# Kernel optimization log

Measured on AMD Instinct MI355X. Metric: run time of the kernel, lower is better.

The kernel has to match this reference:

```python
import jax, jax.numpy as jnp
import numpy as np

B, L, D = 4, 4096, 1024  # batch, seq_len, d_model


def setup_inputs() -> dict:
    key = jax.random.key(0)
    k0, k1, k2 = jax.random.split(key, 3)
    x = jax.random.normal(k0, (B, L, D), dtype=jnp.float32)
    # Dense(d_model*3) applied to x: kernel [D, 3D], bias [3D]
    W_proj = jax.random.normal(k1, (D, 3 * D), dtype=jnp.float32) / np.sqrt(D)
    b_proj = jnp.zeros((3 * D,), dtype=jnp.float32)
    # Output Dense(d_model): kernel [D, D], bias [D]
    W_out = jax.random.normal(k2, (D, D), dtype=jnp.float32) / np.sqrt(D)
    b_out = jnp.zeros((D,), dtype=jnp.float32)
    return {"x": x, "W_proj": W_proj, "b_proj": b_proj,
            "W_out": W_out, "b_out": b_out,
            "layer_idx": 0, "num_layers": 12}


def reference(x, W_proj, b_proj, W_out, b_out, layer_idx, num_layers):
    # x: [B, L, D] -> x_proj: [B, L, 3D]
    x_proj = jnp.einsum('bld,de->ble', x, W_proj) + b_proj
    gate_input, forget_input, output_gate = jnp.split(x_proj, 3, axis=-1)
    # NOTE: in the source, forget_gate / input_gate / k / v / the lax.scan
    # recurrence are defined but never used to produce the output (dead code).
    # The live path is exactly:
    out = gate_input * jax.nn.sigmoid(output_gate)          # [B, L, D]
    out = jnp.einsum('bld,de->ble', out, W_out) + b_out     # [B, L, D]
    # Dropout is deterministic (training=False) -> identity.
    return out
```

## Files before the change

### kernel.cpp

```cpp
#include <hip/hip_runtime.h>
#include <hip/hip_bf16.h>


#define MTOT 16384
#define DM   1024
#define MEG  (1024 * 1024)

typedef __bf16 bf16x8 __attribute__((ext_vector_type(8)));
typedef float  f32x4  __attribute__((ext_vector_type(4)));

#define AS1 __attribute__((address_space(1)))
#define AS3 __attribute__((address_space(3)))

static __device__ __forceinline__ void async_load16(const void* g, void* l) {
    __builtin_amdgcn_global_load_lds((const AS1 void*)g, (AS3 void*)l, 16, 0, 0);
}

static __device__ __forceinline__ unsigned short f2bf(float f) {
    __hip_bfloat16 h = __float2bfloat16(f);
    return *(unsigned short*)&h;
}

__global__ __launch_bounds__(256)
void conv_x(const float* __restrict__ x, unsigned short* __restrict__ dst) {
    const size_t i = ((size_t)blockIdx.x * 256 + threadIdx.x) * 8;
    const f32x4 a = *(const f32x4*)(x + i);
    const f32x4 b = *(const f32x4*)(x + i + 4);
    __align__(16) unsigned short o[8];
    o[0] = f2bf(a[0]); o[1] = f2bf(a[1]); o[2] = f2bf(a[2]); o[3] = f2bf(a[3]);
    o[4] = f2bf(b[0]); o[5] = f2bf(b[1]); o[6] = f2bf(b[2]); o[7] = f2bf(b[3]);
    *(uint4*)(dst + i) = *(const uint4*)o;
}

__global__ void transpose_w(const float* __restrict__ Wproj, const float* __restrict__ Wout,
                            unsigned short* __restrict__ dst0) {
    __shared__ unsigned short t[32][33];
    const int z = blockIdx.z;
    const float* src;
    unsigned short* dst;
    int ld, coff;
    if (z == 0)      { src = Wproj; ld = 3072; coff = 0;    dst = dst0; }
    else if (z == 1) { src = Wproj; ld = 3072; coff = 2048; dst = dst0 + MEG; }
    else             { src = Wout;  ld = 1024; coff = 0;    dst = dst0 + 2 * MEG; }
    const int k0 = blockIdx.x * 32;
    const int n0 = blockIdx.y * 32;
    const int tx = threadIdx.x, ty = threadIdx.y;
    for (int i = ty; i < 32; i += 8)
        t[i][tx] = f2bf(src[(size_t)(k0 + i) * ld + coff + n0 + tx]);
    __syncthreads();
    for (int i = ty; i < 32; i += 8)
        dst[(size_t)(n0 + i) * DM + k0 + tx] = t[tx][i];
}

__global__ __launch_bounds__(512)
void gemm1_fused(const unsigned short* __restrict__ X,
                 const unsigned short* __restrict__ WgT,
                 const unsigned short* __restrict__ WoT,
                 const float* __restrict__ bproj,
                 unsigned short* __restrict__ Hlo,
                 unsigned short* __restrict__ Hhi) {
    __shared__ __align__(16) unsigned short sA[2][256 * 64];
    __shared__ __align__(16) unsigned short sB[2][256 * 64];

    const int tid  = threadIdx.x;
    const int wave = tid >> 6;
    const int lane = tid & 63;
    const int wm = wave & 1;
    const int wn = wave >> 1;

    const int bid = blockIdx.x;
    const int swz = (bid & 7) * 64 + (bid >> 3);
    const int m0 = (swz >> 3) * 256;
    const int n0 = (swz & 7) * 128;

    unsigned short* __restrict__ H =
        (m0 < 8192) ? Hlo : (Hhi - (size_t)8192 * DM);

    const int rA = lane & 15;
    const int qq = lane >> 4;
    const int r7 = rA & 7;
    const int swq   = ((qq ^ (r7 & 3)) << 4);
    const int k0off = ((rA >> 2) & 1) << 6;
    const int k1off = k0off ^ 64;
    const int ldsA_base = (wm * 64 + rA) * 128 + swq;
    const int ldsB_base = (wn * 16 + rA) * 128 + swq;

    const int trow = tid >> 3;
    const int tsw  = (((tid & 7) ^ (trow & 7)) << 4);
    const char* srcA  = (const char*)X   + (size_t)(m0 + trow) * 2048 + tsw;
    const char* srcBg = (const char*)WgT + (size_t)(n0 + trow) * 2048 + tsw;
    const char* srcBo = (const char*)WoT + (size_t)(n0 + trow) * 2048 + tsw;
    char* dA = (char*)&sA[0][0] + tid * 16;
    char* dB = (char*)&sB[0][0] + tid * 16;

#define STA1(b, kt, r)  async_load16(srcA  + (kt) * 128 + (r) * 131072, dA + (b) * 32768 + (r) * 8192)
#define STBG1(b, kt, r) async_load16(srcBg + (kt) * 128 + (r) * 131072, dB + (b) * 32768 + (r) * 8192)
#define STBO1(b, kt, r) async_load16(srcBo + (kt) * 128 + (r) * 131072, dB + (b) * 32768 + (2 + (r)) * 8192)
#define LDA1(dst, bb, h, il, kof) dst = *(const bf16x8*)((const char*)sA + (bb) * 32768 + ldsA_base + (h) * 16384 + (il) * 2048 + (kof))
#define LDB1(dst, bb, mat, j, kof) dst = *(const bf16x8*)((const char*)sB + (bb) * 32768 + ldsB_base + (mat) * 16384 + (j) * 8192 + (kof))

    f32x4 aG[2][4][2], aO[2][4][2];
    bf16x8 fa[4][2], fbg[2][2], fbo[2][2];

    STA1(0, 0, 0); STA1(0, 0, 1); STA1(0, 0, 2); STA1(0, 0, 3);
    STBG1(0, 0, 0); STBG1(0, 0, 1); STBO1(0, 0, 0); STBO1(0, 0, 1);
    STA1(1, 1, 0); STA1(1, 1, 1); STBG1(1, 1, 0); STBO1(1, 1, 0);

#pragma unroll
    for (int h = 0; h < 2; ++h)
#pragma unroll
        for (int il = 0; il < 4; ++il)
#pragma unroll
            for (int jl = 0; jl < 2; ++jl) {
                aG[h][il][jl] = (f32x4){0.f, 0.f, 0.f, 0.f};
                aO[h][il][jl] = (f32x4){0.f, 0.f, 0.f, 0.f};
            }

    asm volatile("s_waitcnt vmcnt(4)" ::: "memory");
    __builtin_amdgcn_s_barrier();

#define MM1(H_) do { \
    _Pragma("unroll") \
    for (int kk = 0; kk < 2; ++kk) \
        _Pragma("unroll") \
        for (int il = 0; il < 4; ++il) \
            _Pragma("unroll") \
            for (int jl = 0; jl < 2; ++jl) { \
                aG[H_][il][jl] = __builtin_amdgcn_mfma_f32_16x16x32_bf16(fa[il][kk], fbg[jl][kk], aG[H_][il][jl], 0, 0, 0); \
                aO[H_][il][jl] = __builtin_amdgcn_mfma_f32_16x16x32_bf16(fa[il][kk], fbo[jl][kk], aO[H_][il][jl], 0, 0, 0); \
            } } while (0)

#define TILE1(kt, b, nb) do { \
    _Pragma("unroll") \
    for (int il = 0; il < 4; ++il) { LDA1(fa[il][0], b, 0, il, k0off); LDA1(fa[il][1], b, 0, il, k1off); } \
    _Pragma("unroll") \
    for (int jl = 0; jl < 2; ++jl) { \
        LDB1(fbg[jl][0], b, 0, jl, k0off); LDB1(fbg[jl][1], b, 0, jl, k1off); \
        LDB1(fbo[jl][0], b, 1, jl, k0off); LDB1(fbo[jl][1], b, 1, jl, k1off); } \
    if ((kt) < 15) { STA1(nb, (kt) + 1, 2); STA1(nb, (kt) + 1, 3); STBG1(nb, (kt) + 1, 1); STBO1(nb, (kt) + 1, 1); } \
    asm volatile("s_waitcnt lgkmcnt(0)" ::: "memory"); \
    __builtin_amdgcn_sched_barrier(0); \
    __builtin_amdgcn_s_setprio(1); MM1(0); __builtin_amdgcn_s_setprio(0); \
    __builtin_amdgcn_s_barrier(); \
    _Pragma("unroll") \
    for (int il = 0; il < 4; ++il) { LDA1(fa[il][0], b, 1, il, k0off); LDA1(fa[il][1], b, 1, il, k1off); } \
    if ((kt) < 14) { STA1(b, (kt) + 2, 0); STA1(b, (kt) + 2, 1); STBG1(b, (kt) + 2, 0); STBO1(b, (kt) + 2, 0); } \
    asm volatile("s_waitcnt lgkmcnt(0)" ::: "memory"); \
    __builtin_amdgcn_sched_barrier(0); \
    __builtin_amdgcn_s_setprio(1); MM1(1); __builtin_amdgcn_s_setprio(0); \
    if ((kt) < 14) { asm volatile("s_waitcnt vmcnt(4)" ::: "memory"); } \
    else           { asm volatile("s_waitcnt vmcnt(0)" ::: "memory"); } \
    __builtin_amdgcn_s_barrier(); \
} while (0)

#pragma unroll 1
    for (int kt2 = 0; kt2 < 16; kt2 += 2) {
        TILE1(kt2, 0, 1);
        TILE1(kt2 + 1, 1, 0);
    }
#undef TILE1
#undef MM1
#undef STA1
#undef STBG1
#undef STBO1
#undef LDA1
#undef LDB1

    const int colL = lane & 15;
    const int rowQ = (lane >> 4) * 4;
#pragma unroll
    for (int jl = 0; jl < 2; ++jl) {
        const int n = n0 + wn * 16 + jl * 64 + colL;
        const float bgv = bproj[n];
        const float bov = bproj[2048 + n];
#pragma unroll
        for (int h = 0; h < 2; ++h)
#pragma unroll
            for (int il = 0; il < 4; ++il) {
                const int mbase = m0 + wm * 64 + h * 128 + il * 16 + rowQ;
#pragma unroll
                for (int r = 0; r < 4; ++r) {
                    const float g = aG[h][il][jl][r] + bgv;
                    const float o = aO[h][il][jl][r] + bov;
                    const float hv = g * (1.0f / (1.0f + __expf(-o)));
                    H[(size_t)(mbase + r) * DM + n] = f2bf(hv);
                }
            }
    }
}

__global__ __launch_bounds__(512)
void gemm2(const unsigned short* __restrict__ Hlo,
           const unsigned short* __restrict__ Hhi,
           const unsigned short* __restrict__ Bt,
           const float* __restrict__ bout,
           float* __restrict__ Out,
           int row_base) {
    __shared__ __align__(16) unsigned short sA[2][256 * 64];
    __shared__ __align__(16) unsigned short sB[2][256 * 64];

    const int tid  = threadIdx.x;
    const int wave = tid >> 6;
    const int lane = tid & 63;
    const int wm = wave & 1;
    const int wn = wave >> 1;

    const int bid = blockIdx.x;
    const int q8  = (int)gridDim.x >> 3;
    const int swz = (bid & 7) * q8 + (bid >> 3);
    const int m0 = row_base + (swz >> 2) * 256;
    const int n0 = (swz & 3) * 256;

    const unsigned short* __restrict__ A =
        (m0 < 8192) ? (Hlo + (size_t)m0 * DM) : (Hhi + (size_t)(m0 - 8192) * DM);

    const int rA = lane & 15;
    const int qq = lane >> 4;
    const int r7 = rA & 7;
    const int swq   = ((qq ^ (r7 & 3)) << 4);
    const int k0off = ((rA >> 2) & 1) << 6;
    const int k1off = k0off ^ 64;
    const int ldsA_base = (wm * 64 + rA) * 128 + swq;
    const int ldsB_base = (wn * 16 + rA) * 128 + swq;

    const int trow = tid >> 3;
    const int tsw  = (((tid & 7) ^ (trow & 7)) << 4);
    const char* srcA = (const char*)A  + (size_t)trow * 2048 + tsw;
    const char* srcB = (const char*)Bt + (size_t)(n0 + trow) * 2048 + tsw;
    char* dA = (char*)&sA[0][0] + tid * 16;
    char* dB = (char*)&sB[0][0] + tid * 16;

#define STA2(b, kt, r) async_load16(srcA + (kt) * 128 + (r) * 131072, dA + (b) * 32768 + (r) * 8192)
#define STB2(b, kt, r) async_load16(srcB + (kt) * 128 + (r) * 131072, dB + (b) * 32768 + (r) * 8192)
#define LDA2(dst, bb, h, il, kof) dst = *(const bf16x8*)((const char*)sA + (bb) * 32768 + ldsA_base + (h) * 16384 + (il) * 2048 + (kof))
#define LDB2(dst, bb, jl, kof)    dst = *(const bf16x8*)((const char*)sB + (bb) * 32768 + ldsB_base + (jl) * 8192 + (kof))

    f32x4 acc[2][4][4];
    bf16x8 fa[4][2], fb[4][2];

    STA2(0, 0, 0); STA2(0, 0, 1); STA2(0, 0, 2); STA2(0, 0, 3);
    STB2(0, 0, 0); STB2(0, 0, 1); STB2(0, 0, 2); STB2(0, 0, 3);
    STA2(1, 1, 0); STA2(1, 1, 1); STB2(1, 1, 0); STB2(1, 1, 1);

#pragma unroll
    for (int h = 0; h < 2; ++h)
#pragma unroll
        for (int il = 0; il < 4; ++il)
#pragma unroll
            for (int jl = 0; jl < 4; ++jl)
                acc[h][il][jl] = (f32x4){0.f, 0.f, 0.f, 0.f};

    asm volatile("s_waitcnt vmcnt(4)" ::: "memory");
    __builtin_amdgcn_s_barrier();

#define MM2(H_) do { \
    _Pragma("unroll") \
    for (int kk = 0; kk < 2; ++kk) \
        _Pragma("unroll") \
        for (int il = 0; il < 4; ++il) \
            _Pragma("unroll") \
            for (int jl = 0; jl < 4; ++jl) \
                acc[H_][il][jl] = __builtin_amdgcn_mfma_f32_16x16x32_bf16(fa[il][kk], fb[jl][kk], acc[H_][il][jl], 0, 0, 0); \
    } while (0)

#define TILE2(kt, b, nb) do { \
     \
    _Pragma("unroll") \
    for (int il = 0; il < 4; ++il) { LDA2(fa[il][0], b, 0, il, k0off); LDA2(fa[il][1], b, 0, il, k1off); } \
    _Pragma("unroll") \
    for (int jl = 0; jl < 4; ++jl) { LDB2(fb[jl][0], b, jl, k0off); LDB2(fb[jl][1], b, jl, k1off); } \
    if ((kt) < 15) { STA2(nb, (kt) + 1, 2); STA2(nb, (kt) + 1, 3); STB2(nb, (kt) + 1, 2); STB2(nb, (kt) + 1, 3); } \
    asm volatile("s_waitcnt lgkmcnt(0)" ::: "memory"); \
    __builtin_amdgcn_sched_barrier(0); \
    __builtin_amdgcn_s_setprio(1); MM2(0); __builtin_amdgcn_s_setprio(0); \
    __builtin_amdgcn_s_barrier(); \
     \
    _Pragma("unroll") \
    for (int il = 0; il < 4; ++il) { LDA2(fa[il][0], b, 1, il, k0off); LDA2(fa[il][1], b, 1, il, k1off); } \
    if ((kt) < 14) { STA2(b, (kt) + 2, 0); STA2(b, (kt) + 2, 1); STB2(b, (kt) + 2, 0); STB2(b, (kt) + 2, 1); } \
    asm volatile("s_waitcnt lgkmcnt(0)" ::: "memory"); \
    __builtin_amdgcn_sched_barrier(0); \
    __builtin_amdgcn_s_setprio(1); MM2(1); __builtin_amdgcn_s_setprio(0); \
    if ((kt) < 14) { asm volatile("s_waitcnt vmcnt(4)" ::: "memory"); } \
    else           { asm volatile("s_waitcnt vmcnt(0)" ::: "memory"); } \
    __builtin_amdgcn_s_barrier(); \
} while (0)

#pragma unroll 1
    for (int kt2 = 0; kt2 < 16; kt2 += 2) {
        TILE2(kt2, 0, 1);
        TILE2(kt2 + 1, 1, 0);
    }
#undef TILE2
#undef MM2
#undef STA2
#undef STB2
#undef LDA2
#undef LDB2

    const int colL = lane & 15;
    const int rowQ = (lane >> 4) * 4;
#pragma unroll
    for (int jl = 0; jl < 4; ++jl) {
        const int n = n0 + wn * 16 + jl * 64 + colL;
        const float bv = bout[n];
#pragma unroll
        for (int h = 0; h < 2; ++h)
#pragma unroll
            for (int il = 0; il < 4; ++il) {
                const int mbase = m0 + wm * 64 + h * 128 + il * 16 + rowQ;
#pragma unroll
                for (int r = 0; r < 4; ++r)
                    Out[(size_t)(mbase + r) * DM + n] = acc[h][il][jl][r] + bv;
            }
    }
}

extern "C" void kernel_launch(void* const* d_in, const int* in_sizes, int n_in,
                              void* d_out, int out_size, void* d_ws, size_t ws_size,
                              hipStream_t stream) {
    const float* x     = (const float*)d_in[0];
    const float* Wproj = (const float*)d_in[1];
    const float* bproj = (const float*)d_in[2];
    const float* Wout  = (const float*)d_in[3];
    const float* bout  = (const float*)d_in[4];
    float* out = (float*)d_out;

    unsigned short* Xb  = (unsigned short*)d_out;
    unsigned short* WgT   = (unsigned short*)d_ws;
    unsigned short* WoT   = WgT + MEG;
    unsigned short* WoutT = WgT + 2 * MEG;
    unsigned short* Hws   = WgT + 3 * MEG;

    const bool big_ws = ws_size >= (size_t)19 * MEG * 2;

    unsigned short* Hlo = big_ws ? Hws : ((unsigned short*)d_out + 16 * MEG);
    unsigned short* Hhi = big_ws ? (Hws + (size_t)8192 * DM) : Hws;

    conv_x<<<(MTOT * DM) / (256 * 8), 256, 0, stream>>>(x, Xb);

    transpose_w<<<dim3(32, 32, 3), dim3(32, 8, 1), 0, stream>>>(Wproj, Wout, WgT);

    gemm1_fused<<<512, 512, 0, stream>>>(Xb, WgT, WoT, bproj, Hlo, Hhi);

    if (big_ws) {
        gemm2<<<256, 512, 0, stream>>>(Hlo, Hhi, WoutT, bout, out, 0);
    } else {
        gemm2<<<128, 512, 0, stream>>>(Hlo, Hhi, WoutT, bout, out, 0);
        gemm2<<<128, 512, 0, stream>>>(Hlo, Hhi, WoutT, bout, out, 8192);
    }
}
```

Baseline: 238.9 us.

## Merge prep kernels and add 128x128-tile gemm2 variant for small workspace

Fuses the bf16 conversion of x and the weight transpose into one launch, removing a kernel launch and its dependency gap. Adds a gemm2_small kernel with 128x128 tiles and 256 threads, used when the workspace is too small for the 256-block path. That gives each half-launch 512 blocks instead of 128, filling more CUs at the cost of less data reuse per tile. The big-workspace gemm2 keeps its grid hardcoded to 256 blocks.

```diff
diff --git a/kernel.cpp b/kernel.cpp
--- a/kernel.cpp
+++ b/kernel.cpp
@@ -22,29 +22,34 @@
 }
 
 __global__ __launch_bounds__(256)
-void conv_x(const float* __restrict__ x, unsigned short* __restrict__ dst) {
-    const size_t i = ((size_t)blockIdx.x * 256 + threadIdx.x) * 8;
-    const f32x4 a = *(const f32x4*)(x + i);
-    const f32x4 b = *(const f32x4*)(x + i + 4);
-    __align__(16) unsigned short o[8];
-    o[0] = f2bf(a[0]); o[1] = f2bf(a[1]); o[2] = f2bf(a[2]); o[3] = f2bf(a[3]);
-    o[4] = f2bf(b[0]); o[5] = f2bf(b[1]); o[6] = f2bf(b[2]); o[7] = f2bf(b[3]);
-    *(uint4*)(dst + i) = *(const uint4*)o;
-}
-
-__global__ void transpose_w(const float* __restrict__ Wproj, const float* __restrict__ Wout,
-                            unsigned short* __restrict__ dst0) {
+void prep(const float* __restrict__ x, const float* __restrict__ Wproj,
+          const float* __restrict__ Wout,
+          unsigned short* __restrict__ Xb, unsigned short* __restrict__ Wdst) {
     __shared__ unsigned short t[32][33];
-    const int z = blockIdx.z;
+    const int bid = blockIdx.x;
+    const int tid = threadIdx.x;
+    if (bid < 8192) {
+        const size_t i = ((size_t)bid * 256 + tid) * 8;
+        const f32x4 a = *(const f32x4*)(x + i);
+        const f32x4 b = *(const f32x4*)(x + i + 4);
+        __align__(16) unsigned short o[8];
+        o[0] = f2bf(a[0]); o[1] = f2bf(a[1]); o[2] = f2bf(a[2]); o[3] = f2bf(a[3]);
+        o[4] = f2bf(b[0]); o[5] = f2bf(b[1]); o[6] = f2bf(b[2]); o[7] = f2bf(b[3]);
+        *(uint4*)(Xb + i) = *(const uint4*)o;
+        return;
+    }
+    const int bid2 = bid - 8192;
+    const int z  = bid2 >> 10;
+    const int rem = bid2 & 1023;
+    const int k0 = (rem & 31) * 32;
+    const int n0 = (rem >> 5) * 32;
     const float* src;
     unsigned short* dst;
     int ld, coff;
-    if (z == 0)      { src = Wproj; ld = 3072; coff = 0;    dst = dst0; }
-    else if (z == 1) { src = Wproj; ld = 3072; coff = 2048; dst = dst0 + MEG; }
-    else             { src = Wout;  ld = 1024; coff = 0;    dst = dst0 + 2 * MEG; }
-    const int k0 = blockIdx.x * 32;
-    const int n0 = blockIdx.y * 32;
-    const int tx = threadIdx.x, ty = threadIdx.y;
+    if (z == 0)      { src = Wproj; ld = 3072; coff = 0;    dst = Wdst; }
+    else if (z == 1) { src = Wproj; ld = 3072; coff = 2048; dst = Wdst + MEG; }
+    else             { src = Wout;  ld = 1024; coff = 0;    dst = Wdst + 2 * MEG; }
+    const int tx = tid & 31, ty = tid >> 5;
     for (int i = ty; i < 32; i += 8)
         t[i][tx] = f2bf(src[(size_t)(k0 + i) * ld + coff + n0 + tx]);
     __syncthreads();
@@ -190,12 +195,11 @@
 }
 
 __global__ __launch_bounds__(512)
-void gemm2(const unsigned short* __restrict__ Hlo,
-           const unsigned short* __restrict__ Hhi,
-           const unsigned short* __restrict__ Bt,
-           const float* __restrict__ bout,
-           float* __restrict__ Out,
-           int row_base) {
+void gemm2_big(const unsigned short* __restrict__ Hlo,
+               const unsigned short* __restrict__ Hhi,
+               const unsigned short* __restrict__ Bt,
+               const float* __restrict__ bout,
+               float* __restrict__ Out) {
     __shared__ __align__(16) unsigned short sA[2][256 * 64];
     __shared__ __align__(16) unsigned short sB[2][256 * 64];
 
@@ -206,9 +210,8 @@
     const int wn = wave >> 1;
 
     const int bid = blockIdx.x;
-    const int q8  = (int)gridDim.x >> 3;
-    const int swz = (bid & 7) * q8 + (bid >> 3);
-    const int m0 = row_base + (swz >> 2) * 256;
+    const int swz = (bid & 7) * 32 + (bid >> 3);
+    const int m0 = (swz >> 2) * 256;
     const int n0 = (swz & 3) * 256;
 
     const unsigned short* __restrict__ A =
@@ -264,7 +267,6 @@
     } while (0)
 
 #define TILE2(kt, b, nb) do { \
-     \
     _Pragma("unroll") \
     for (int il = 0; il < 4; ++il) { LDA2(fa[il][0], b, 0, il, k0off); LDA2(fa[il][1], b, 0, il, k1off); } \
     _Pragma("unroll") \
@@ -274,7 +276,6 @@
     __builtin_amdgcn_sched_barrier(0); \
     __builtin_amdgcn_s_setprio(1); MM2(0); __builtin_amdgcn_s_setprio(0); \
     __builtin_amdgcn_s_barrier(); \
-     \
     _Pragma("unroll") \
     for (int il = 0; il < 4; ++il) { LDA2(fa[il][0], b, 1, il, k0off); LDA2(fa[il][1], b, 1, il, k1off); } \
     if ((kt) < 14) { STA2(b, (kt) + 2, 0); STA2(b, (kt) + 2, 1); STB2(b, (kt) + 2, 0); STB2(b, (kt) + 2, 1); } \
@@ -313,6 +314,125 @@
                 for (int r = 0; r < 4; ++r)
                     Out[(size_t)(mbase + r) * DM + n] = acc[h][il][jl][r] + bv;
             }
+    }
+}
+
+__global__ __launch_bounds__(256)
+void gemm2_small(const unsigned short* __restrict__ Hlo,
+                 const unsigned short* __restrict__ Hhi,
+                 const unsigned short* __restrict__ Bt,
+                 const float* __restrict__ bout,
+                 float* __restrict__ Out,
+                 int row_base) {
+    __shared__ __align__(16) unsigned short sA[2][128 * 64];
+    __shared__ __align__(16) unsigned short sB[2][128 * 64];
+
+    const int tid  = threadIdx.x;
+    const int wave = tid >> 6;
+    const int lane = tid & 63;
+    const int wm = wave & 1;
+    const int wn = wave >> 1;
+
+    const int bid = blockIdx.x;
+    const int q8  = (int)gridDim.x >> 3;
+    const int swz = (bid & 7) * q8 + (bid >> 3);
+    const int m0 = row_base + (swz >> 3) * 128;
+    const int n0 = (swz & 7) * 128;
+
+    const unsigned short* __restrict__ A =
+        (m0 < 8192) ? (Hlo + (size_t)m0 * DM) : (Hhi + (size_t)(m0 - 8192) * DM);
+
+    const int rA = lane & 15;
+    const int qq = lane >> 4;
+    const int r7 = rA & 7;
+    const int swq   = ((qq ^ (r7 & 3)) << 4);
+    const int k0off = ((rA >> 2) & 1) << 6;
+    const int k1off = k0off ^ 64;
+    const int ldsA_base = (wm * 64 + rA) * 128 + swq;
+    const int ldsB_base = (wn * 64 + rA) * 128 + swq;
+
+    const int trow = tid >> 3;
+    const int tsw  = (((tid & 7) ^ (trow & 7)) << 4);
+    const char* srcA = (const char*)A  + (size_t)trow * 2048 + tsw;
+    const char* srcB = (const char*)Bt + (size_t)(n0 + trow) * 2048 + tsw;
+    char* dA = (char*)&sA[0][0] + tid * 16;
+    char* dB = (char*)&sB[0][0] + tid * 16;
+
+#define STA3(b, kt, r) async_load16(srcA + (kt) * 128 + (r) * 65536, dA + (b) * 16384 + (r) * 4096)
+#define STB3(b, kt, r) async_load16(srcB + (kt) * 128 + (r) * 65536, dB + (b) * 16384 + (r) * 4096)
+#define LDA3(dst, bb, il, kof) dst = *(const bf16x8*)((const char*)sA + (bb) * 16384 + ldsA_base + (il) * 2048 + (kof))
+#define LDB3(dst, bb, jl, kof) dst = *(const bf16x8*)((const char*)sB + (bb) * 16384 + ldsB_base + (jl) * 2048 + (kof))
+
+    f32x4 acc[4][4];
+    bf16x8 fa[4][2], fb[4][2];
+
+    STA3(0, 0, 0); STA3(0, 0, 1); STA3(0, 0, 2); STA3(0, 0, 3);
+    STB3(0, 0, 0); STB3(0, 0, 1); STB3(0, 0, 2); STB3(0, 0, 3);
+    STA3(1, 1, 0); STA3(1, 1, 1); STB3(1, 1, 0); STB3(1, 1, 2);
+
+#pragma unroll
+    for (int il = 0; il < 4; ++il)
+#pragma unroll
+        for (int j = 0; j < 4; ++j) acc[il][j] = (f32x4){0.f, 0.f, 0.f, 0.f};
+
+    asm volatile("s_waitcnt vmcnt(4)" ::: "memory");
+    __builtin_amdgcn_s_barrier();
+
+#define MM3(JB) do { \
+    _Pragma("unroll") \
+    for (int kk = 0; kk < 2; ++kk) \
+        _Pragma("unroll") \
+        for (int il = 0; il < 4; ++il) { \
+            acc[il][JB]     = __builtin_amdgcn_mfma_f32_16x16x32_bf16(fa[il][kk], fb[JB][kk],     acc[il][JB],     0, 0, 0); \
+            acc[il][JB + 1] = __builtin_amdgcn_mfma_f32_16x16x32_bf16(fa[il][kk], fb[JB + 1][kk], acc[il][JB + 1], 0, 0, 0); \
+        } } while (0)
+
+#define TILE3(kt, b, nb) do { \
+    _Pragma("unroll") \
+    for (int il = 0; il < 4; ++il) { LDA3(fa[il][0], b, il, k0off); LDA3(fa[il][1], b, il, k1off); } \
+    _Pragma("unroll") \
+    for (int jl = 0; jl < 2; ++jl) { LDB3(fb[jl][0], b, jl, k0off); LDB3(fb[jl][1], b, jl, k1off); } \
+    if ((kt) < 15) { STA3(nb, (kt) + 1, 2); STA3(nb, (kt) + 1, 3); STB3(nb, (kt) + 1, 1); STB3(nb, (kt) + 1, 3); } \
+    asm volatile("s_waitcnt lgkmcnt(0)" ::: "memory"); \
+    __builtin_amdgcn_sched_barrier(0); \
+    __builtin_amdgcn_s_setprio(1); MM3(0); __builtin_amdgcn_s_setprio(0); \
+    __builtin_amdgcn_s_barrier(); \
+    _Pragma("unroll") \
+    for (int jl = 2; jl < 4; ++jl) { LDB3(fb[jl][0], b, jl, k0off); LDB3(fb[jl][1], b, jl, k1off); } \
+    if ((kt) < 14) { STA3(b, (kt) + 2, 0); STA3(b, (kt) + 2, 1); STB3(b, (kt) + 2, 0); STB3(b, (kt) + 2, 2); } \
+    asm volatile("s_waitcnt lgkmcnt(0)" ::: "memory"); \
+    __builtin_amdgcn_sched_barrier(0); \
+    __builtin_amdgcn_s_setprio(1); MM3(2); __builtin_amdgcn_s_setprio(0); \
+    if ((kt) < 14) { asm volatile("s_waitcnt vmcnt(4)" ::: "memory"); } \
+    else           { asm volatile("s_waitcnt vmcnt(0)" ::: "memory"); } \
+    __builtin_amdgcn_s_barrier(); \
+} while (0)
+
+#pragma unroll 1
+    for (int kt2 = 0; kt2 < 16; kt2 += 2) {
+        TILE3(kt2, 0, 1);
+        TILE3(kt2 + 1, 1, 0);
+    }
+#undef TILE3
+#undef MM3
+#undef STA3
+#undef STB3
+#undef LDA3
+#undef LDB3
+
+    const int colL = lane & 15;
+    const int rowQ = (lane >> 4) * 4;
+#pragma unroll
+    for (int jl = 0; jl < 4; ++jl) {
+        const int n = n0 + wn * 64 + jl * 16 + colL;
+        const float bv = bout[n];
+#pragma unroll
+        for (int il = 0; il < 4; ++il) {
+            const int mbase = m0 + wm * 64 + il * 16 + rowQ;
+#pragma unroll
+            for (int r = 0; r < 4; ++r)
+                Out[(size_t)(mbase + r) * DM + n] = acc[il][jl][r] + bv;
+        }
     }
 }
 
@@ -328,7 +448,6 @@
 
     unsigned short* Xb  = (unsigned short*)d_out;
     unsigned short* WgT   = (unsigned short*)d_ws;
-    unsigned short* WoT   = WgT + MEG;
     unsigned short* WoutT = WgT + 2 * MEG;
     unsigned short* Hws   = WgT + 3 * MEG;
 
@@ -337,16 +456,14 @@
     unsigned short* Hlo = big_ws ? Hws : ((unsigned short*)d_out + 16 * MEG);
     unsigned short* Hhi = big_ws ? (Hws + (size_t)8192 * DM) : Hws;
 
-    conv_x<<<(MTOT * DM) / (256 * 8), 256, 0, stream>>>(x, Xb);
-
-    transpose_w<<<dim3(32, 32, 3), dim3(32, 8, 1), 0, stream>>>(Wproj, Wout, WgT);
-
-    gemm1_fused<<<512, 512, 0, stream>>>(Xb, WgT, WoT, bproj, Hlo, Hhi);
+    prep<<<8192 + 3072, 256, 0, stream>>>(x, Wproj, Wout, Xb, WgT);
+
+    gemm1_fused<<<512, 512, 0, stream>>>(Xb, WgT, WgT + MEG, bproj, Hlo, Hhi);
 
     if (big_ws) {
-        gemm2<<<256, 512, 0, stream>>>(Hlo, Hhi, WoutT, bout, out, 0);
+        gemm2_big<<<256, 512, 0, stream>>>(Hlo, Hhi, WoutT, bout, out);
     } else {
-        gemm2<<<128, 512, 0, stream>>>(Hlo, Hhi, WoutT, bout, out, 0);
-        gemm2<<<128, 512, 0, stream>>>(Hlo, Hhi, WoutT, bout, out, 8192);
-    }
-}
+        gemm2_small<<<512, 256, 0, stream>>>(Hlo, Hhi, WoutT, bout, out, 0);
+        gemm2_small<<<512, 256, 0, stream>>>(Hlo, Hhi, WoutT, bout, out, 8192);
+    }
+}
```

Result: faster. 231.1 us (-3.3%).
